# Kernel optimization log

Hardware: AMD Instinct MI355X
Metric: run time of the kernel (lower is better)

Reference implementation:

```python
import jax, jax.numpy as jnp
import numpy as np

EPS = 1e-8  # torch F.cosine_similarity default eps


def setup_inputs() -> dict:
    key = jax.random.key(0)
    k1, k2 = jax.random.split(key)
    xs_pad = jax.random.normal(k1, (8, 4096, 512), dtype=jnp.float32)
    spk_emb = jax.random.normal(k2, (8, 256, 512), dtype=jnp.float32)
    return {"xs_pad": xs_pad, "spk_emb": spk_emb}


def reference(xs_pad, spk_emb):
    # Faithful to F.cosine_similarity(x.unsqueeze(2), y.unsqueeze(1), dim=-1):
    #   dot(x, y) / (max(||x||, eps) * max(||y||, eps))
    # Implemented as L2-normalize then a batched GEMM -> (B, T, S), avoiding
    # the (B, T, S, D) broadcast intermediate.
    x_norm = jnp.maximum(jnp.linalg.norm(xs_pad, axis=-1, keepdims=True), EPS)
    y_norm = jnp.maximum(jnp.linalg.norm(spk_emb, axis=-1, keepdims=True), EPS)
    xn = xs_pad / x_norm          # (B, T, D)
    yn = spk_emb / y_norm         # (B, S, D)
    scores = jnp.einsum('btd,bsd->bts', xn, yn)  # (B, T, S)
    return scores
```

## Files before the change

### kernel.cpp

```cpp
#include <hip/hip_runtime.h>
#include <hip/hip_bf16.h>

#define BB 8
#define TT 4096
#define SS 256
#define DD 512

typedef __attribute__((ext_vector_type(8))) short short8;
typedef __attribute__((ext_vector_type(4))) float floatx4;
typedef __attribute__((ext_vector_type(4))) int intx4;

__device__ inline int pk2(float a, float b) {
  __hip_bfloat162 h = __float22bfloat162_rn(make_float2(a, b));
  int r;
  __builtin_memcpy(&r, &h, 4);
  return r;
}

__device__ inline short8 cvt8(float4 f0, float4 f1) {
  intx4 p;
  p[0] = pk2(f0.x, f0.y);
  p[1] = pk2(f0.z, f0.w);
  p[2] = pk2(f1.x, f1.y);
  p[3] = pk2(f1.z, f1.w);
  return __builtin_bit_cast(short8, p);
}

__global__ __launch_bounds__(256) void cos_packB_kernel(
    const float* __restrict__ spk, short* __restrict__ bp) {
  const int idx = blockIdx.x;
  const int b = idx >> 3;
  const int tn = (idx >> 2) & 1;
  const int kh = idx & 3;
  const int tid = threadIdx.x;
  short* dst = bp + (size_t)idx * 2048 * 8;
#pragma unroll
  for (int j = 0; j < 8; j++) {
    int u = j * 256 + tid;
    int row = u >> 4;
    int kblk = (u & 15) ^ (row & 15);
    const float* src =
        spk + ((size_t)(b * SS + tn * 128 + row)) * DD + kh * 128 + kblk * 8;
    float4 f0 = *(const float4*)src;
    float4 f1 = *(const float4*)(src + 4);
    short8 o = cvt8(f0, f1);
    *(short8*)(dst + (size_t)u * 8) = o;
  }
}

__global__ __launch_bounds__(256) void cos_fused_kernel(
    const float* __restrict__ xs, const short* __restrict__ bp,
    float* __restrict__ out) {
  __shared__ float sA[128 * 64];
  __shared__ short sB[128 * 128];
  __shared__ float scX[128];
  __shared__ float scY[128];

  const int tid = threadIdx.x;
  const int wave = tid >> 6;
  const int lane = tid & 63;
  const int tn = blockIdx.x;
  const int tm = blockIdx.y;
  const int b = blockIdx.z;

  const float* Abase = xs + ((size_t)b * TT + tm * 128) * DD;
  const short* Bbase = bp + ((size_t)(b * 2 + tn) * 4) * 2048 * 8;

  floatx4 acc[4][4];
#pragma unroll
  for (int i = 0; i < 4; i++)
#pragma unroll
    for (int j = 0; j < 4; j++) acc[i][j] = (floatx4){0.f, 0.f, 0.f, 0.f};
  floatx4 accG[4];
#pragma unroll
  for (int i = 0; i < 4; i++) accG[i] = (floatx4){0.f, 0.f, 0.f, 0.f};

  const int wm = wave >> 1;
  const int wn = wave & 1;
  const int quad = lane >> 4;
  const int l15 = lane & 15;
  const bool gramA = (wm == wn);

  int aoff[8];
#pragma unroll
  for (int j = 0; j < 8; j++) {
    int s = j * 256 + tid;
    int row = s >> 4;
    int blk = (s & 15) ^ (row & 15);
    aoff[j] = row * DD + blk * 4;
  }

  for (int kt = 0; kt < DD / 64; ++kt) {
    if ((kt & 1) == 0) {
      const short* gB = Bbase + (size_t)(kt >> 1) * 2048 * 8;
#pragma unroll
      for (int j = 0; j < 8; j++) {
        __builtin_amdgcn_global_load_lds(
            (const __attribute__((address_space(1))) unsigned int*)(gB +
                (size_t)(j * 256 + wave * 64 + lane) * 8),
            (__attribute__((address_space(3))) unsigned int*)(sB +
                (size_t)(j * 256 + wave * 64) * 8),
            16, 0, 0);
      }
    }
#pragma unroll
    for (int j = 0; j < 8; j++) {
      __builtin_amdgcn_global_load_lds(
          (const __attribute__((address_space(1))) unsigned int*)(Abase +
              aoff[j] + kt * 64),
          (__attribute__((address_space(3))) unsigned int*)(sA +
              (j * 256 + wave * 64) * 4),
          16, 0, 0);
    }
    __syncthreads();

#pragma unroll
    for (int ks = 0; ks < 2; ks++) {
      short8 af[4], bfr[4];
      const int b0s = ks * 8 + quad * 2;
      const int bslot = (kt & 1) * 8 + ks * 4 + quad;
#pragma unroll
      for (int im = 0; im < 4; im++) {
        int row = wm * 64 + im * 16 + l15;
        int s0 = b0s ^ (row & 15);
        int s1 = (b0s + 1) ^ (row & 15);
        float4 f0 = *(const float4*)(sA + row * 64 + s0 * 4);
        float4 f1 = *(const float4*)(sA + row * 64 + s1 * 4);
        af[im] = cvt8(f0, f1);
      }
#pragma unroll
      for (int in = 0; in < 4; in++) {
        int row = wn * 64 + in * 16 + l15;
        int s = bslot ^ (row & 15);
        bfr[in] = *(const short8*)(sB + row * 128 + s * 8);
      }
#pragma unroll
      for (int im = 0; im < 4; im++)
#pragma unroll
        for (int in = 0; in < 4; in++)
          acc[im][in] = __builtin_amdgcn_mfma_f32_16x16x32_bf16(
              af[im], bfr[in], acc[im][in], 0, 0, 0);
      if (gramA) {
#pragma unroll
        for (int im = 0; im < 4; im++)
          accG[im] = __builtin_amdgcn_mfma_f32_16x16x32_bf16(
              af[im], af[im], accG[im], 0, 0, 0);
      } else {
#pragma unroll
        for (int in = 0; in < 4; in++)
          accG[in] = __builtin_amdgcn_mfma_f32_16x16x32_bf16(
              bfr[in], bfr[in], accG[in], 0, 0, 0);
      }
    }
    __syncthreads();
  }

  if (quad == (l15 >> 2)) {
#pragma unroll
    for (int i = 0; i < 4; i++) {
      float inv = 1.0f / fmaxf(sqrtf(accG[i][l15 & 3]), 1e-8f);
      if (gramA)
        scX[wm * 64 + i * 16 + l15] = inv;
      else
        scY[wn * 64 + i * 16 + l15] = inv;
    }
  }
  __syncthreads();

  float* Obase = out + ((size_t)b * TT + tm * 128) * SS + tn * 128;
#pragma unroll
  for (int im = 0; im < 4; im++) {
#pragma unroll
    for (int in = 0; in < 4; in++) {
      int col = wn * 64 + in * 16 + l15;
      float yv = scY[col];
#pragma unroll
      for (int r = 0; r < 4; r++) {
        int row = wm * 64 + im * 16 + quad * 4 + r;
        Obase[row * SS + col] = acc[im][in][r] * scX[row] * yv;
      }
    }
  }
}

extern "C" void kernel_launch(void* const* d_in, const int* in_sizes, int n_in,
                              void* d_out, int out_size, void* d_ws,
                              size_t ws_size, hipStream_t stream) {
  const float* xs = (const float*)d_in[0];
  const float* spk = (const float*)d_in[1];
  float* out = (float*)d_out;
  short* bp = (short*)d_ws;

  hipLaunchKernelGGL(cos_packB_kernel, dim3(64), dim3(256), 0, stream, spk,
                     bp);
  hipLaunchKernelGGL(cos_fused_kernel, dim3(SS / 128, TT / 128, BB), dim3(256),
                     0, stream, xs, bp, out);
}
```

Baseline: 117.4 us.

## Prepack B into MFMA fragment order, double-buffer A in LDS, XCD-aware block mapping

The pack kernel now writes spk_emb in per-wave MFMA fragment order, so the main kernel loads B operands straight from global memory into registers instead of staging them through LDS. The A tile in LDS is double-buffered, so the next k-step's async global-to-LDS load overlaps with compute, and one barrier per step replaces two. A 1D grid is remapped so blocks sharing the same batch and row tile land on the same XCD for L2 reuse. The costs are more global-load latency exposed on the B path and a larger LDS footprint for A, which may lower occupancy.

```diff
diff --git a/kernel.cpp b/kernel.cpp
--- a/kernel.cpp
+++ b/kernel.cpp
@@ -28,52 +28,43 @@
 
 __global__ __launch_bounds__(256) void cos_packB_kernel(
     const float* __restrict__ spk, short* __restrict__ bp) {
-  const int idx = blockIdx.x;
-  const int b = idx >> 3;
-  const int tn = (idx >> 2) & 1;
-  const int kh = idx & 3;
-  const int tid = threadIdx.x;
-  short* dst = bp + (size_t)idx * 2048 * 8;
-#pragma unroll
-  for (int j = 0; j < 8; j++) {
-    int u = j * 256 + tid;
-    int row = u >> 4;
-    int kblk = (u & 15) ^ (row & 15);
-    const float* src =
-        spk + ((size_t)(b * SS + tn * 128 + row)) * DD + kh * 128 + kblk * 8;
-    float4 f0 = *(const float4*)src;
-    float4 f1 = *(const float4*)(src + 4);
-    short8 o = cvt8(f0, f1);
-    *(short8*)(dst + (size_t)u * 8) = o;
-  }
+  const int id = blockIdx.x;
+  const int ks = id & 1;
+  const int kt = (id >> 1) & 7;
+  const int wn = (id >> 4) & 1;
+  const int tn = (id >> 5) & 1;
+  const int b = id >> 6;
+  const int t = threadIdx.x;
+  const int in = t >> 6;
+  const int lane = t & 63;
+  const int row = tn * 128 + wn * 64 + in * 16 + (lane & 15);
+  const int k = kt * 64 + ks * 32 + (lane >> 4) * 8;
+  const float* src = spk + ((size_t)(b * SS + row)) * DD + k;
+  float4 f0 = *(const float4*)src;
+  float4 f1 = *(const float4*)(src + 4);
+  short8 o = cvt8(f0, f1);
+  size_t frag = (size_t)((((b * 2 + tn) * 2 + wn) * 8 + kt) * 2 + ks) * 4 + in;
+  *(short8*)(bp + frag * 512 + (size_t)lane * 8) = o;
 }
 
 __global__ __launch_bounds__(256) void cos_fused_kernel(
     const float* __restrict__ xs, const short* __restrict__ bp,
     float* __restrict__ out) {
-  __shared__ float sA[128 * 64];
-  __shared__ short sB[128 * 128];
-  __shared__ float scX[128];
-  __shared__ float scY[128];
+  __shared__ float sA[2 * 128 * 64];
+  float* scX = sA;
+  float* scY = sA + 128;
 
   const int tid = threadIdx.x;
   const int wave = tid >> 6;
   const int lane = tid & 63;
-  const int tn = blockIdx.x;
-  const int tm = blockIdx.y;
-  const int b = blockIdx.z;
-
-  const float* Abase = xs + ((size_t)b * TT + tm * 128) * DD;
-  const short* Bbase = bp + ((size_t)(b * 2 + tn) * 4) * 2048 * 8;
-
-  floatx4 acc[4][4];
-#pragma unroll
-  for (int i = 0; i < 4; i++)
-#pragma unroll
-    for (int j = 0; j < 4; j++) acc[i][j] = (floatx4){0.f, 0.f, 0.f, 0.f};
-  floatx4 accG[4];
-#pragma unroll
-  for (int i = 0; i < 4; i++) accG[i] = (floatx4){0.f, 0.f, 0.f, 0.f};
+
+  const int id = blockIdx.x;
+  const int xcd = id & 7;
+  const int j = id >> 3;
+  const int pairIdx = xcd * 32 + (j >> 1);
+  const int tn = j & 1;
+  const int tm = pairIdx & 31;
+  const int b = pairIdx >> 5;
 
   const int wm = wave >> 1;
   const int wn = wave & 1;
@@ -81,65 +72,82 @@
   const int l15 = lane & 15;
   const bool gramA = (wm == wn);
 
+  const float* Abase = xs + ((size_t)b * TT + tm * 128) * DD;
+  const short* Bw =
+      bp + (size_t)((b * 2 + tn) * 2 + wn) * 32768 + (size_t)lane * 8;
+
+  floatx4 acc[4][4];
+#pragma unroll
+  for (int i = 0; i < 4; i++)
+#pragma unroll
+    for (int jj = 0; jj < 4; jj++) acc[i][jj] = (floatx4){0.f, 0.f, 0.f, 0.f};
+  floatx4 accG[4];
+#pragma unroll
+  for (int i = 0; i < 4; i++) accG[i] = (floatx4){0.f, 0.f, 0.f, 0.f};
+
   int aoff[8];
 #pragma unroll
-  for (int j = 0; j < 8; j++) {
-    int s = j * 256 + tid;
+  for (int jj = 0; jj < 8; jj++) {
+    int s = jj * 256 + tid;
     int row = s >> 4;
     int blk = (s & 15) ^ (row & 15);
-    aoff[j] = row * DD + blk * 4;
-  }
-
-  for (int kt = 0; kt < DD / 64; ++kt) {
-    if ((kt & 1) == 0) {
-      const short* gB = Bbase + (size_t)(kt >> 1) * 2048 * 8;
-#pragma unroll
-      for (int j = 0; j < 8; j++) {
+    aoff[jj] = row * DD + blk * 4;
+  }
+
+#pragma unroll
+  for (int jj = 0; jj < 8; jj++) {
+    __builtin_amdgcn_global_load_lds(
+        (const __attribute__((address_space(1))) unsigned int*)(Abase +
+            aoff[jj]),
+        (__attribute__((address_space(3))) unsigned int*)(sA +
+            (jj * 256 + wave * 64) * 4),
+        16, 0, 0);
+  }
+  __syncthreads();
+
+  for (int kt = 0; kt < 8; ++kt) {
+    const int cur = kt & 1;
+
+    short8 breg[2][4];
+    const short* Bkt = Bw + kt * 4096;
+#pragma unroll
+    for (int ksl = 0; ksl < 2; ksl++)
+#pragma unroll
+      for (int in = 0; in < 4; in++)
+        breg[ksl][in] = *(const short8*)(Bkt + ksl * 2048 + in * 512);
+
+    if (kt < 7) {
+#pragma unroll
+      for (int jj = 0; jj < 8; jj++) {
         __builtin_amdgcn_global_load_lds(
-            (const __attribute__((address_space(1))) unsigned int*)(gB +
-                (size_t)(j * 256 + wave * 64 + lane) * 8),
-            (__attribute__((address_space(3))) unsigned int*)(sB +
-                (size_t)(j * 256 + wave * 64) * 8),
+            (const __attribute__((address_space(1))) unsigned int*)(Abase +
+                aoff[jj] + (kt + 1) * 64),
+            (__attribute__((address_space(3))) unsigned int*)(sA +
+                (cur ^ 1) * 8192 + (jj * 256 + wave * 64) * 4),
             16, 0, 0);
       }
     }
-#pragma unroll
-    for (int j = 0; j < 8; j++) {
-      __builtin_amdgcn_global_load_lds(
-          (const __attribute__((address_space(1))) unsigned int*)(Abase +
-              aoff[j] + kt * 64),
-          (__attribute__((address_space(3))) unsigned int*)(sA +
-              (j * 256 + wave * 64) * 4),
-          16, 0, 0);
-    }
-    __syncthreads();
-
+
+    const float* sAc = sA + cur * 8192;
 #pragma unroll
     for (int ks = 0; ks < 2; ks++) {
-      short8 af[4], bfr[4];
+      short8 af[4];
       const int b0s = ks * 8 + quad * 2;
-      const int bslot = (kt & 1) * 8 + ks * 4 + quad;
 #pragma unroll
       for (int im = 0; im < 4; im++) {
         int row = wm * 64 + im * 16 + l15;
         int s0 = b0s ^ (row & 15);
         int s1 = (b0s + 1) ^ (row & 15);
-        float4 f0 = *(const float4*)(sA + row * 64 + s0 * 4);
-        float4 f1 = *(const float4*)(sA + row * 64 + s1 * 4);
+        float4 f0 = *(const float4*)(sAc + row * 64 + s0 * 4);
+        float4 f1 = *(const float4*)(sAc + row * 64 + s1 * 4);
         af[im] = cvt8(f0, f1);
-      }
-#pragma unroll
-      for (int in = 0; in < 4; in++) {
-        int row = wn * 64 + in * 16 + l15;
-        int s = bslot ^ (row & 15);
-        bfr[in] = *(const short8*)(sB + row * 128 + s * 8);
       }
 #pragma unroll
       for (int im = 0; im < 4; im++)
 #pragma unroll
         for (int in = 0; in < 4; in++)
           acc[im][in] = __builtin_amdgcn_mfma_f32_16x16x32_bf16(
-              af[im], bfr[in], acc[im][in], 0, 0, 0);
+              af[im], breg[ks][in], acc[im][in], 0, 0, 0);
       if (gramA) {
 #pragma unroll
         for (int im = 0; im < 4; im++)
@@ -149,7 +157,7 @@
 #pragma unroll
         for (int in = 0; in < 4; in++)
           accG[in] = __builtin_amdgcn_mfma_f32_16x16x32_bf16(
-              bfr[in], bfr[in], accG[in], 0, 0, 0);
+              breg[ks][in], breg[ks][in], accG[in], 0, 0, 0);
       }
     }
     __syncthreads();
@@ -191,8 +199,8 @@
   float* out = (float*)d_out;
   short* bp = (short*)d_ws;
 
-  hipLaunchKernelGGL(cos_packB_kernel, dim3(64), dim3(256), 0, stream, spk,
+  hipLaunchKernelGGL(cos_packB_kernel, dim3(512), dim3(256), 0, stream, spk,
                      bp);
-  hipLaunchKernelGGL(cos_fused_kernel, dim3(SS / 128, TT / 128, BB), dim3(256),
-                     0, stream, xs, bp, out);
-}
+  hipLaunchKernelGGL(cos_fused_kernel, dim3(512), dim3(256), 0, stream, xs,
+                     bp, out);
+}
```

After: 117.6 us (median of 2 runs). Within noise of the previous version (+0.3%).
